# Kernel tuning notes

Measured on AMD Instinct MI355X. Metric: run time of the kernel, lower is better.

## Reference

```python
import jax, jax.numpy as jnp
import numpy as np
import math

D_MSA, N_HEAD, D_HID = 256, 8, 32
B, N, L = 1, 256, 384


def _xavier(key, shape):
    fan_in, fan_out = shape[1], shape[0]
    a = math.sqrt(6.0 / (fan_in + fan_out))
    return jax.random.uniform(key, shape, jnp.float32, -a, a)


def setup_inputs() -> dict:
    key = jax.random.key(0)
    ks = jax.random.split(key, 8)
    hd = N_HEAD * D_HID
    return {
        "msa": jax.random.normal(ks[0], (B, N, L, D_MSA), jnp.float32),
        "ln_w": jnp.ones((D_MSA,), jnp.float32),
        "ln_b": jnp.zeros((D_MSA,), jnp.float32),
        # torch Linear weight is [out, in]; y = x @ W.T
        "wq": _xavier(ks[1], (hd, D_MSA)),
        "wk": _xavier(ks[2], (hd, D_MSA)),
        "wv": _xavier(ks[3], (hd, D_MSA)),
        # to_g init: zeros weight, ones bias -> randomize a bit for nontrivial test
        "wg": 0.02 * jax.random.normal(ks[4], (hd, D_MSA), jnp.float32),
        "bg": jnp.ones((hd,), jnp.float32),
        "wo": 0.02 * jax.random.normal(ks[5], (D_MSA, hd), jnp.float32),
        "bo": jnp.zeros((D_MSA,), jnp.float32),
    }


def reference(msa, ln_w, ln_b, wq, wk, wv, wg, bg, wo, bo):
    h, d = N_HEAD, D_HID
    scaling = 1.0 / math.sqrt(d)
    b, n, l, dm = msa.shape

    # LayerNorm over last dim
    mu = jnp.mean(msa, axis=-1, keepdims=True)
    var = jnp.var(msa, axis=-1, keepdims=True)
    x = (msa - mu) / jnp.sqrt(var + 1e-5) * ln_w + ln_b

    q = (x @ wq.T).reshape(b, n, l, h, d) * scaling
    k = (x @ wk.T).reshape(b, n, l, h, d)
    v = (x @ wv.T).reshape(b, n, l, h, d)
    gate = jax.nn.sigmoid(x @ wg.T + bg)  # [b,n,l,h*d]

    # column-wise attention: softmax over MSA sequence axis N (keys)
    attn = jnp.einsum("bqihd,bkihd->bihqk", q, k)  # [b,l,h,n,n]
    attn = jax.nn.softmax(attn, axis=-1)
    out = jnp.einsum("bihqk,bkihd->bqihd", attn, v).reshape(b, n, l, h * d)
    out = gate * out
    return out @ wo.T + bo
```

## Files before the change

kernel.cpp:

```cpp
#include <hip/hip_runtime.h>

typedef unsigned short u16;
typedef unsigned int u32;
typedef __attribute__((ext_vector_type(8))) short bf16x8;
typedef __attribute__((ext_vector_type(4))) float f32x4;
typedef __attribute__((ext_vector_type(4))) u32 u32x4;

#define N_SEQ 256
#define L_RES 384
#define DM 256
#define NH 8
#define DH 32
#define M_ROWS (N_SEQ*L_RES)
#define PANEL 8192


__device__ __forceinline__ u16 f2b(float f){
    unsigned u = __builtin_bit_cast(unsigned, f);
    u = u + 0x7fffu + ((u >> 16) & 1u);
    return (u16)(u >> 16);
}
__device__ __forceinline__ float b2f(u16 b){
    unsigned u = ((unsigned)b) << 16;
    return __builtin_bit_cast(float, u);
}
__device__ __forceinline__ u32 pk2(float lo, float hi){
    u32 a = (__builtin_bit_cast(u32, lo) + 0x8000u) >> 16;
    u32 b = (__builtin_bit_cast(u32, hi) + 0x8000u) & 0xffff0000u;
    return a | b;
}
__device__ __forceinline__ int swzB(int a){
    return a ^ (((a>>6)&7)<<3);
}

__global__ __launch_bounds__(256) void k_wcvt(const float* __restrict__ wq,
        const float* __restrict__ wk, const float* __restrict__ wv,
        const float* __restrict__ wg, const float* __restrict__ wo,
        u16* __restrict__ wsw){
    const int mat = blockIdx.x >> 6;
    const float* W = (mat==0)?wq:(mat==1)?wk:(mat==2)?wv:(mat==3)?wg:wo;
    const int r = ((blockIdx.x & 63)*256 + threadIdx.x)*4;
    const int col = r >> 8, k0 = r & 255;
    float4 f = *(const float4*)&W[r];
    ushort4 o;
    o.x = f2b(f.x); o.y = f2b(f.y); o.z = f2b(f.z); o.w = f2b(f.w);
    const int off = ((col>>4)*32 + (k0>>3))*128 + (col&15)*8 + (k0&7);
    *(ushort4*)&wsw[mat*65536 + off] = o;
}

__global__ __launch_bounds__(256) void k_ln(const float* __restrict__ msa,
        const float* __restrict__ lnw, const float* __restrict__ lnb,
        u16* __restrict__ xo){
    const int tid = threadIdx.x;
    const int r16 = tid >> 4, lane16 = tid & 15;
    const size_t row = (size_t)blockIdx.x*16 + r16;
    const float4* src = (const float4*)(msa + row*DM + lane16*16);
    float4 a[4];
    float s = 0.f, ss = 0.f;
    #pragma unroll
    for(int j=0;j<4;j++){
        a[j] = src[j];
        s  += a[j].x + a[j].y + a[j].z + a[j].w;
        ss += a[j].x*a[j].x + a[j].y*a[j].y + a[j].z*a[j].z + a[j].w*a[j].w;
    }
    #pragma unroll
    for(int m=1;m<16;m<<=1){ s += __shfl_xor(s,m); ss += __shfl_xor(ss,m); }
    const float mu  = s*(1.f/DM);
    const float inv = rsqrtf(ss*(1.f/DM) - mu*mu + 1e-5f);
    const float4* wv4 = (const float4*)(lnw + lane16*16);
    const float4* bv4 = (const float4*)(lnb + lane16*16);
    u32 pk[8];
    #pragma unroll
    for(int j=0;j<4;j++){
        float4 w = wv4[j], b = bv4[j];
        float e0 = (a[j].x-mu)*inv*w.x + b.x;
        float e1 = (a[j].y-mu)*inv*w.y + b.y;
        float e2 = (a[j].z-mu)*inv*w.z + b.z;
        float e3 = (a[j].w-mu)*inv*w.w + b.w;
        pk[j*2]   = (u32)f2b(e0) | ((u32)f2b(e1)<<16);
        pk[j*2+1] = (u32)f2b(e2) | ((u32)f2b(e3)<<16);
    }
    u16* base = xo + (size_t)blockIdx.x*4096 + lane16*256 + r16*8;
    *(uint4*)base       = *(uint4*)&pk[0];
    *(uint4*)(base+128) = *(uint4*)&pk[4];
}

__global__ __launch_bounds__(512) void k_qkvg(const u16* __restrict__ x,
        const u16* __restrict__ wsw, const float* __restrict__ bg,
        u16* __restrict__ qo, u16* __restrict__ ko,
        u16* __restrict__ vo, u16* __restrict__ go){
    __shared__ __align__(16) u16 Bs[16384];
    const int cb = blockIdx.x, by = blockIdx.y;
    const int mat = cb >> 2, c0 = (cb&3)*64;
    const int tid = threadIdx.x;
    const u16* wt = wsw + mat*65536 + (c0>>4)*4096;
    #pragma unroll
    for(int i=0;i<4;i++)
        *(uint4*)&Bs[swzB(i*4096 + tid*8)] = *(const uint4*)&wt[i*4096 + tid*8];
    const int w = tid>>6, lane = tid&63, l15 = lane&15, lq = lane>>4;
    const u16* xa = x + ((size_t)by*8 + w)*4096;
    bf16x8 xf[8];
    #pragma unroll
    for(int kk=0;kk<8;kk++)
        xf[kk] = *(const bf16x8*)&xa[(kk*4+lq)*128 + l15*8];
    __syncthreads();
    f32x4 acc[4] = {};
    #pragma unroll
    for(int kk=0;kk<8;kk++){
        #pragma unroll
        for(int nt=0;nt<4;nt++){
            bf16x8 b = *(const bf16x8*)&Bs[swzB(nt*4096 + (kk*4+lq)*128 + l15*8)];
            acc[nt] = __builtin_amdgcn_mfma_f32_16x16x32_bf16(b,xf[kk],acc[nt],0,0,0);
        }
    }
    const float scaling = 0.17677669529663687f * 1.44269504088896f;
    u16* O = (mat==0)?qo:(mat==1)?ko:(mat==2)?vo:go;
    const int n0 = by/3, l0 = (by%3)*128;
    const int l = l0 + w*16 + l15;
    #pragma unroll
    for(int nt=0;nt<4;nt++){
        const int c = c0 + nt*16 + lq*4;
        float v0 = acc[nt][0], v1 = acc[nt][1];
        float v2 = acc[nt][2], v3 = acc[nt][3];
        if(mat==0){ v0*=scaling; v1*=scaling; v2*=scaling; v3*=scaling; }
        else if(mat==3){
            const float4 bgv = *(const float4*)&bg[c];
            v0 = 1.f/(1.f+__expf(-(v0+bgv.x)));
            v1 = 1.f/(1.f+__expf(-(v1+bgv.y)));
            v2 = 1.f/(1.f+__expf(-(v2+bgv.z)));
            v3 = 1.f/(1.f+__expf(-(v3+bgv.w)));
        }
        uint2 ov;
        ov.x = pk2(v0, v1);
        ov.y = pk2(v2, v3);
        const int h2 = c >> 5, d = c & 31;
        *(uint2*)&O[((size_t)l*NH + h2)*PANEL + n0*32 + d] = ov;
    }
}

__global__ __launch_bounds__(512, 4) void k_attn(const u16* __restrict__ q,
        const u16* __restrict__ k, const u16* __restrict__ v,
        const u16* __restrict__ g, u16* __restrict__ ao){
    __shared__ __align__(16) u16 KFs[8192];
    __shared__ __align__(16) u16 VFs[8192];
    const int h = blockIdx.x, l = blockIdx.y;
    const int tid = threadIdx.x;
    const size_t pbase = ((size_t)l*NH + h)*PANEL;
    const u16* kp = k + pbase;
    const u16* vp = v + pbase;
    #pragma unroll
    for(int j=0;j<2;j++){
        const int u = j*512 + tid;
        const int key = u>>2, dblk = u&3;
        const uint4 tk = *(const uint4*)&kp[u*8];
        *(uint4*)&KFs[((key>>4)*4 + dblk)*128 + (key&15)*8] = tk;
        const uint4 tv = *(const uint4*)&vp[u*8];
        const int T = key>>4, gg = (key>>2)&3, r = key&3;
        const int pkey = (T>>1)*32 + ((gg&2)|(T&1))*8 + r + (((gg^T)&1)<<2);
        const int plo = (pkey>>3)*128 + (pkey&7);
        const u32 wv_[4] = {tv.x, tv.y, tv.z, tv.w};
        #pragma unroll
        for(int wd=0; wd<4; wd++){
            const int d_lo = dblk*8 + wd*2, d_hi = d_lo+1;
            VFs[((d_lo)>>4)*4096 + plo + ((d_lo)&15)*8] = (u16)(wv_[wd]&0xffff);
            VFs[((d_hi)>>4)*4096 + plo + ((d_hi)&15)*8] = (u16)(wv_[wd]>>16);
        }
    }
    __syncthreads();
    const int w = tid>>6, lane = tid&63;
    const int l15 = lane&15, lq = lane>>4;
    const int lodd = lq & 1;
    const u16* qp = q + pbase;
    const u16* gp = g + pbase;
    u16* aop = ao + pbase;
    const int q0a = w*32, q0b = w*32 + 16;
    const bf16x8 bqA = *(const bf16x8*)&qp[(q0a+l15)*32 + lq*8];
    const bf16x8 bqB = *(const bf16x8*)&qp[(q0b+l15)*32 + lq*8];
    float mA = -1e30f, spA = 0.f;
    float mB = -1e30f, spB = 0.f;
    f32x4 oaccA[2] = {}, oaccB[2] = {};
    #pragma unroll
    for(int ch=0; ch<4; ch++){
        f32x4 sA[4], sB[4];
        #pragma unroll
        for(int tt=0;tt<4;tt++){
            bf16x8 ak = *(const bf16x8*)&KFs[((ch*4+tt)*4 + lq)*128 + l15*8];
            f32x4 z = {};
            sA[tt] = __builtin_amdgcn_mfma_f32_16x16x32_bf16(ak,bqA,z,0,0,0);
            f32x4 z2 = {};
            sB[tt] = __builtin_amdgcn_mfma_f32_16x16x32_bf16(ak,bqB,z2,0,0,0);
        }
        float cmA = fmaxf(fmaxf(fmaxf(sA[0][0],sA[0][1]),fmaxf(sA[0][2],sA[0][3])),
                   fmaxf(fmaxf(fmaxf(sA[1][0],sA[1][1]),fmaxf(sA[1][2],sA[1][3])),
                   fmaxf(fmaxf(fmaxf(sA[2][0],sA[2][1]),fmaxf(sA[2][2],sA[2][3])),
                         fmaxf(fmaxf(sA[3][0],sA[3][1]),fmaxf(sA[3][2],sA[3][3])))));
        float cmB = fmaxf(fmaxf(fmaxf(sB[0][0],sB[0][1]),fmaxf(sB[0][2],sB[0][3])),
                   fmaxf(fmaxf(fmaxf(sB[1][0],sB[1][1]),fmaxf(sB[1][2],sB[1][3])),
                   fmaxf(fmaxf(fmaxf(sB[2][0],sB[2][1]),fmaxf(sB[2][2],sB[2][3])),
                         fmaxf(fmaxf(sB[3][0],sB[3][1]),fmaxf(sB[3][2],sB[3][3])))));
        cmA = fmaxf(cmA, __shfl_xor(cmA,16));
        cmB = fmaxf(cmB, __shfl_xor(cmB,16));
        cmA = fmaxf(cmA, __shfl_xor(cmA,32));
        cmB = fmaxf(cmB, __shfl_xor(cmB,32));
        const float mnA = fmaxf(mA, cmA), mnB = fmaxf(mB, cmB);
        const float scA = exp2f(mA - mnA), scB = exp2f(mB - mnB);
        mA = mnA; mB = mnB;
        float csA = 0.f, csB = 0.f;
        #pragma unroll
        for(int tt=0;tt<4;tt++){
            #pragma unroll
            for(int rg=0;rg<4;rg++){
                float eA = exp2f(sA[tt][rg] - mnA);
                float eB = exp2f(sB[tt][rg] - mnB);
                sA[tt][rg] = eA; csA += eA;
                sB[tt][rg] = eB; csB += eB;
            }
        }
        spA = spA*scA + csA;
        spB = spB*scB + csB;
        #pragma unroll
        for(int i=0;i<4;i++){ oaccA[0][i]*=scA; oaccA[1][i]*=scA; oaccB[0][i]*=scB; oaccB[1][i]*=scB; }
        #pragma unroll
        for(int half=0; half<2; half++){
            const int mwin = ch*2 + half;
            u32 eA0 = pk2(sA[half*2][0],   sA[half*2][1]);
            u32 eA1 = pk2(sA[half*2][2],   sA[half*2][3]);
            u32 oA0 = pk2(sA[half*2+1][0], sA[half*2+1][1]);
            u32 oA1 = pk2(sA[half*2+1][2], sA[half*2+1][3]);
            u32 eB0 = pk2(sB[half*2][0],   sB[half*2][1]);
            u32 eB1 = pk2(sB[half*2][2],   sB[half*2][3]);
            u32 oB0 = pk2(sB[half*2+1][0], sB[half*2+1][1]);
            u32 oB1 = pk2(sB[half*2+1][2], sB[half*2+1][3]);
            u32 ownA0 = lodd ? oA0 : eA0,  ownA1 = lodd ? oA1 : eA1;
            u32 sndA0 = lodd ? eA0 : oA0,  sndA1 = lodd ? eA1 : oA1;
            u32 ownB0 = lodd ? oB0 : eB0,  ownB1 = lodd ? oB1 : eB1;
            u32 sndB0 = lodd ? eB0 : oB0,  sndB1 = lodd ? eB1 : oB1;
            u32 rcA0 = (u32)__shfl_xor((int)sndA0, 16);
            u32 rcB0 = (u32)__shfl_xor((int)sndB0, 16);
            u32 rcA1 = (u32)__shfl_xor((int)sndA1, 16);
            u32 rcB1 = (u32)__shfl_xor((int)sndB1, 16);
            u32x4 pwA = {ownA0, ownA1, rcA0, rcA1};
            u32x4 pwB = {ownB0, ownB1, rcB0, rcB1};
            bf16x8 pfA = __builtin_bit_cast(bf16x8, pwA);
            bf16x8 pfB = __builtin_bit_cast(bf16x8, pwB);
            #pragma unroll
            for(int nt=0;nt<2;nt++){
                bf16x8 av = *(const bf16x8*)&VFs[(nt*32 + mwin*4 + lq)*128 + l15*8];
                oaccA[nt] = __builtin_amdgcn_mfma_f32_16x16x32_bf16(av,pfA,oaccA[nt],0,0,0);
                oaccB[nt] = __builtin_amdgcn_mfma_f32_16x16x32_bf16(av,pfB,oaccB[nt],0,0,0);
            }
        }
    }
    spA += __shfl_xor(spA, 16);
    spB += __shfl_xor(spB, 16);
    spA += __shfl_xor(spA, 32);
    spB += __shfl_xor(spB, 32);
    const float rinvA = 1.f/spA, rinvB = 1.f/spB;
    const int qnA = q0a + l15, qnB = q0b + l15;
    #pragma unroll
    for(int nt=0;nt<2;nt++){
        const int c = nt*16 + lq*4;
        const uint2 glA = *(const uint2*)&gp[qnA*32 + c];
        const uint2 glB = *(const uint2*)&gp[qnB*32 + c];
        uint2 ovA, ovB;
        ovA.x = pk2(b2f((u16)(glA.x&0xffff))*oaccA[nt][0]*rinvA,
                    b2f((u16)(glA.x>>16))   *oaccA[nt][1]*rinvA);
        ovA.y = pk2(b2f((u16)(glA.y&0xffff))*oaccA[nt][2]*rinvA,
                    b2f((u16)(glA.y>>16))   *oaccA[nt][3]*rinvA);
        ovB.x = pk2(b2f((u16)(glB.x&0xffff))*oaccB[nt][0]*rinvB,
                    b2f((u16)(glB.x>>16))   *oaccB[nt][1]*rinvB);
        ovB.y = pk2(b2f((u16)(glB.y&0xffff))*oaccB[nt][2]*rinvB,
                    b2f((u16)(glB.y>>16))   *oaccB[nt][3]*rinvB);
        *(uint2*)&aop[qnA*32 + c] = ovA;
        *(uint2*)&aop[qnB*32 + c] = ovB;
    }
}

__global__ __launch_bounds__(512) void k_out(const u16* __restrict__ a,
        const u16* __restrict__ wsw, const float* __restrict__ bo,
        float* __restrict__ out){
    __shared__ __align__(16) u16 Bs[16384];
    const int cb = blockIdx.x, nb = blockIdx.y, l = blockIdx.z;
    const int c0 = cb*64;
    const int tid = threadIdx.x;
    const u16* wt = wsw + 4*65536 + (c0>>4)*4096;
    #pragma unroll
    for(int i=0;i<4;i++)
        *(uint4*)&Bs[swzB(i*4096 + tid*8)] = *(const uint4*)&wt[i*4096 + tid*8];
    const int w = tid>>6, lane = tid&63, l15 = lane&15, lq = lane>>4;
    const int n0 = nb*128 + w*16;
    const size_t lbase = (size_t)l*NH*PANEL;
    bf16x8 af[8];
    #pragma unroll
    for(int kk=0;kk<8;kk++)
        af[kk] = *(const bf16x8*)&a[lbase + (size_t)kk*PANEL + (n0 + l15)*32 + lq*8];
    __syncthreads();
    f32x4 acc[4] = {};
    #pragma unroll
    for(int kk=0;kk<8;kk++){
        #pragma unroll
        for(int nt=0;nt<4;nt++){
            bf16x8 b = *(const bf16x8*)&Bs[swzB(nt*4096 + (kk*4+lq)*128 + l15*8)];
            acc[nt] = __builtin_amdgcn_mfma_f32_16x16x32_bf16(af[kk],b,acc[nt],0,0,0);
        }
    }
    #pragma unroll
    for(int nt=0;nt<4;nt++){
        const int c = c0 + nt*16 + l15;
        const float bov = bo[c];
        #pragma unroll
        for(int rg=0;rg<4;rg++){
            const int n = n0 + lq*4 + rg;
            out[((size_t)n*L_RES + l)*DM + c] = acc[nt][rg] + bov;
        }
    }
}

extern "C" void kernel_launch(void* const* d_in, const int* in_sizes, int n_in,
                              void* d_out, int out_size, void* d_ws, size_t ws_size,
                              hipStream_t stream){
    const float* msa = (const float*)d_in[0];
    const float* lnw = (const float*)d_in[1];
    const float* lnb = (const float*)d_in[2];
    const float* wq  = (const float*)d_in[3];
    const float* wk  = (const float*)d_in[4];
    const float* wv  = (const float*)d_in[5];
    const float* wg  = (const float*)d_in[6];
    const float* bg  = (const float*)d_in[7];
    const float* wo  = (const float*)d_in[8];
    const float* bo  = (const float*)d_in[9];
    float* out = (float*)d_out;

    const size_t SEG = (size_t)M_ROWS * DM;
    u16 *xs, *qs, *ks, *vs, *gs, *aos, *wsw;
    if (ws_size >= (6*SEG + 5*65536) * sizeof(u16)) {
        xs  = (u16*)d_ws;
        qs  = xs + SEG;
        ks  = qs + SEG;
        vs  = ks + SEG;
        gs  = vs + SEG;
        aos = gs + SEG;
        wsw = aos + SEG;
    } else {
        xs  = (u16*)d_ws;
        qs  = xs + SEG;
        gs  = qs + SEG;
        wsw = gs + SEG;
        ks  = (u16*)d_out;
        vs  = ks + SEG;
        aos = xs;
    }

    k_wcvt<<<320, 256, 0, stream>>>(wq, wk, wv, wg, wo, wsw);
    k_ln  <<<M_ROWS/16, 256, 0, stream>>>(msa, lnw, lnb, xs);
    k_qkvg<<<dim3(16, M_ROWS/128), 512, 0, stream>>>(xs, wsw, bg, qs, ks, vs, gs);
    k_attn<<<dim3(NH, L_RES), 512, 0, stream>>>(qs, ks, vs, gs, aos);
    k_out <<<dim3(4, 2, L_RES), 512, 0, stream>>>(aos, wsw, bo, out);
}
```

Before: 290.9 us.

## Switch QKVG projection to 32x32x16 MFMA with new weight layout

The QKVG projection kernel now uses 32x32x16 bf16 MFMA tiles instead of 16x16x32, with 4 waves each handling 32 rows by 64 columns. The weight preconversion writes Q/K/V/G weights in a new layout that matches this tile shape, and the LDS swizzle is dropped. X fragments are streamed from global memory inside the k-loop instead of being preloaded into registers. The aim is fewer LDS reads per FLOP and higher MFMA efficiency. The trade-offs are a smaller block (256 threads), unswizzled LDS accesses that may cause bank conflicts, and per-iteration global loads.

```diff
diff --git a/kernel.cpp b/kernel.cpp
--- a/kernel.cpp
+++ b/kernel.cpp
@@ -4,6 +4,7 @@
 typedef unsigned int u32;
 typedef __attribute__((ext_vector_type(8))) short bf16x8;
 typedef __attribute__((ext_vector_type(4))) float f32x4;
+typedef __attribute__((ext_vector_type(16))) float f32x16;
 typedef __attribute__((ext_vector_type(4))) u32 u32x4;
 
 #define N_SEQ 256
@@ -44,7 +45,11 @@
     float4 f = *(const float4*)&W[r];
     ushort4 o;
     o.x = f2b(f.x); o.y = f2b(f.y); o.z = f2b(f.z); o.w = f2b(f.w);
-    const int off = ((col>>4)*32 + (k0>>3))*128 + (col&15)*8 + (k0&7);
+    int off;
+    if(mat < 4)
+        off = (col>>5)*8192 + (k0>>4)*512 + ((k0>>3)&1)*256 + (col&31)*8 + (k0&7);
+    else
+        off = ((col>>4)*32 + (k0>>3))*128 + (col&15)*8 + (k0&7);
     *(ushort4*)&wsw[mat*65536 + off] = o;
 }
 
@@ -85,56 +90,58 @@
     *(uint4*)(base+128) = *(uint4*)&pk[4];
 }
 
-__global__ __launch_bounds__(512) void k_qkvg(const u16* __restrict__ x,
+__global__ __launch_bounds__(256) void k_qkvg(const u16* __restrict__ x,
         const u16* __restrict__ wsw, const float* __restrict__ bg,
         u16* __restrict__ qo, u16* __restrict__ ko,
         u16* __restrict__ vo, u16* __restrict__ go){
-    __shared__ __align__(16) u16 Bs[16384];
+    __shared__ __align__(16) u16 Ws[16384];
     const int cb = blockIdx.x, by = blockIdx.y;
     const int mat = cb >> 2, c0 = (cb&3)*64;
     const int tid = threadIdx.x;
-    const u16* wt = wsw + mat*65536 + (c0>>4)*4096;
-    #pragma unroll
-    for(int i=0;i<4;i++)
-        *(uint4*)&Bs[swzB(i*4096 + tid*8)] = *(const uint4*)&wt[i*4096 + tid*8];
-    const int w = tid>>6, lane = tid&63, l15 = lane&15, lq = lane>>4;
-    const u16* xa = x + ((size_t)by*8 + w)*4096;
-    bf16x8 xf[8];
-    #pragma unroll
-    for(int kk=0;kk<8;kk++)
-        xf[kk] = *(const bf16x8*)&xa[(kk*4+lq)*128 + l15*8];
+    const u16* wt = wsw + mat*65536 + (c0>>5)*8192;
+    #pragma unroll
+    for(int i=0;i<8;i++)
+        *(uint4*)&Ws[i*2048 + tid*8] = *(const uint4*)&wt[i*2048 + tid*8];
     __syncthreads();
-    f32x4 acc[4] = {};
-    #pragma unroll
-    for(int kk=0;kk<8;kk++){
-        #pragma unroll
-        for(int nt=0;nt<4;nt++){
-            bf16x8 b = *(const bf16x8*)&Bs[swzB(nt*4096 + (kk*4+lq)*128 + l15*8)];
-            acc[nt] = __builtin_amdgcn_mfma_f32_16x16x32_bf16(b,xf[kk],acc[nt],0,0,0);
+    const int w = tid>>6, lane = tid&63;
+    const int r31 = lane&31, hi = lane>>5;
+    const int rb = by*128 + w*32;
+    const u16* xb = x + ((size_t)(rb>>4) + (r31>>4))*4096 + (r31&15)*8 + hi*128;
+    f32x16 acc[2] = {};
+    #pragma unroll
+    for(int ks=0;ks<16;ks++){
+        bf16x8 bx = *(const bf16x8*)&xb[ks*256];
+        #pragma unroll
+        for(int ct=0;ct<2;ct++){
+            bf16x8 aw = *(const bf16x8*)&Ws[ct*8192 + ks*512 + hi*256 + r31*8];
+            acc[ct] = __builtin_amdgcn_mfma_f32_32x32x16_bf16(aw,bx,acc[ct],0,0,0);
         }
     }
     const float scaling = 0.17677669529663687f * 1.44269504088896f;
     u16* O = (mat==0)?qo:(mat==1)?ko:(mat==2)?vo:go;
     const int n0 = by/3, l0 = (by%3)*128;
-    const int l = l0 + w*16 + l15;
-    #pragma unroll
-    for(int nt=0;nt<4;nt++){
-        const int c = c0 + nt*16 + lq*4;
-        float v0 = acc[nt][0], v1 = acc[nt][1];
-        float v2 = acc[nt][2], v3 = acc[nt][3];
-        if(mat==0){ v0*=scaling; v1*=scaling; v2*=scaling; v3*=scaling; }
-        else if(mat==3){
-            const float4 bgv = *(const float4*)&bg[c];
-            v0 = 1.f/(1.f+__expf(-(v0+bgv.x)));
-            v1 = 1.f/(1.f+__expf(-(v1+bgv.y)));
-            v2 = 1.f/(1.f+__expf(-(v2+bgv.z)));
-            v3 = 1.f/(1.f+__expf(-(v3+bgv.w)));
-        }
-        uint2 ov;
-        ov.x = pk2(v0, v1);
-        ov.y = pk2(v2, v3);
-        const int h2 = c >> 5, d = c & 31;
-        *(uint2*)&O[((size_t)l*NH + h2)*PANEL + n0*32 + d] = ov;
+    const int lrow = l0 + w*32 + r31;
+    #pragma unroll
+    for(int ct=0;ct<2;ct++){
+        #pragma unroll
+        for(int t=0;t<4;t++){
+            const int c = c0 + ct*32 + t*8 + hi*4;
+            float v0 = acc[ct][4*t+0], v1 = acc[ct][4*t+1];
+            float v2 = acc[ct][4*t+2], v3 = acc[ct][4*t+3];
+            if(mat==0){ v0*=scaling; v1*=scaling; v2*=scaling; v3*=scaling; }
+            else if(mat==3){
+                const float4 bgv = *(const float4*)&bg[c];
+                v0 = 1.f/(1.f+__expf(-(v0+bgv.x)));
+                v1 = 1.f/(1.f+__expf(-(v1+bgv.y)));
+                v2 = 1.f/(1.f+__expf(-(v2+bgv.z)));
+                v3 = 1.f/(1.f+__expf(-(v3+bgv.w)));
+            }
+            uint2 ov;
+            ov.x = pk2(v0, v1);
+            ov.y = pk2(v2, v3);
+            const int h2 = c >> 5, d = c & 31;
+            *(uint2*)&O[((size_t)lrow*NH + h2)*PANEL + n0*32 + d] = ov;
+        }
     }
 }
 
@@ -353,7 +360,7 @@
 
     k_wcvt<<<320, 256, 0, stream>>>(wq, wk, wv, wg, wo, wsw);
     k_ln  <<<M_ROWS/16, 256, 0, stream>>>(msa, lnw, lnb, xs);
-    k_qkvg<<<dim3(16, M_ROWS/128), 512, 0, stream>>>(xs, wsw, bg, qs, ks, vs, gs);
+    k_qkvg<<<dim3(16, M_ROWS/128), 256, 0, stream>>>(xs, wsw, bg, qs, ks, vs, gs);
     k_attn<<<dim3(NH, L_RES), 512, 0, stream>>>(qs, ks, vs, gs, aos);
     k_out <<<dim3(4, 2, L_RES), 512, 0, stream>>>(aos, wsw, bo, out);
 }
```

Measured after the change: 310.6 us. +6.8%, slower.
